# Kernel tuning notes

Measured on AMD Instinct MI355X. Metric: run time of the kernel, lower is better.

The kernel has to match this reference:

```python
import jax, jax.numpy as jnp
import numpy as np

D_MODEL, D_K, D_V, H = 512, 64, 64, 8
B, NQ, NK = 16, 784, 784
HW = 28  # sqrt(NQ)


def setup_inputs() -> dict:
    key = jax.random.key(0)
    ks = jax.random.split(key, 12)
    std = 0.001  # torch init.normal_(weight, std=0.001)
    return {
        "queries": jax.random.normal(ks[0], (B, NQ, D_MODEL), jnp.float32),
        "keys": jax.random.normal(ks[1], (B, NK, D_MODEL), jnp.float32),
        "values": jax.random.normal(ks[2], (B, NK, D_MODEL), jnp.float32),
        "self_corr": jax.random.normal(ks[3], (B, 1, NQ, NK), jnp.float32),
        # weights stored [in, out] for x @ W
        "Wq": jax.random.normal(ks[4], (D_MODEL, H * D_K), jnp.float32) * std,
        "bq": jnp.zeros((H * D_K,), jnp.float32),
        "Wk": jax.random.normal(ks[5], (D_MODEL, H * D_K), jnp.float32) * std,
        "bk": jnp.zeros((H * D_K,), jnp.float32),
        "Wv": jax.random.normal(ks[6], (D_MODEL, H * D_V), jnp.float32) * std,
        "bv": jnp.zeros((H * D_V,), jnp.float32),
        "Wo": jax.random.normal(ks[7], (H * D_V, D_MODEL), jnp.float32) * std,
        "bo": jnp.zeros((D_MODEL,), jnp.float32),
    }


def reference(queries, keys, values, self_corr, Wq, bq, Wk, bk, Wv, bv, Wo, bo):
    b, nq, cc = queries.shape
    nk = keys.shape[1]
    # projections -> [b, h, n, d]
    q = (queries @ Wq + bq).reshape(b, nq, H, D_K).transpose(0, 2, 1, 3)
    k = (keys @ Wk + bk).reshape(b, nk, H, D_K).transpose(0, 2, 1, 3)
    v = (values @ Wv + bv).reshape(b, nk, H, D_V).transpose(0, 2, 1, 3)
    # scaled scores [b, h, nq, nk]
    att_qk = jnp.einsum("bhqd,bhkd->bhqk", q, k) / np.sqrt(D_K).astype(np.float32)
    enhanced = att_qk + self_corr.reshape(b, -1, nq, nk)  # additive bias (broadcast over heads)
    attn = jax.nn.softmax(enhanced, axis=-1)
    # dropout is identity at inference (reference in eval mode)
    ctx = jnp.einsum("bhqk,bhkd->bhqd", attn, v)
    ctx = ctx.transpose(0, 2, 1, 3).reshape(b, nq, H * D_V)
    out = ctx @ Wo + bo  # [b, nq, d_model]
    hw = int(np.sqrt(nq))
    return out.transpose(0, 2, 1).reshape(b, cc, hw, hw)
```

## Files before the change

kernel.cpp:

```cpp
#include <hip/hip_runtime.h>

#define SZX ((size_t)12544 * 512)
#define WSEG ((size_t)262144)

typedef __attribute__((ext_vector_type(8))) short short8;
typedef __attribute__((ext_vector_type(4))) short short4s;
typedef __attribute__((ext_vector_type(4))) float floatx4;

typedef const __attribute__((address_space(1))) void* gas_cvp;
typedef __attribute__((address_space(3))) void* las_vp;

__device__ __forceinline__ void gl_lds16(const void* g, void* l) {
    __builtin_amdgcn_global_load_lds((gas_cvp)g, (las_vp)l, 16, 0, 0);
}

__device__ __forceinline__ unsigned short f2bf(float f) {
    unsigned int u = __float_as_uint(f);
    u += 0x7fffu + ((u >> 16) & 1u);
    return (unsigned short)(u >> 16);
}

__device__ __forceinline__ short8 cvt8(floatx4 a, floatx4 b) {
    short8 r;
    r[0] = (short)f2bf(a[0]); r[1] = (short)f2bf(a[1]);
    r[2] = (short)f2bf(a[2]); r[3] = (short)f2bf(a[3]);
    r[4] = (short)f2bf(b[0]); r[5] = (short)f2bf(b[1]);
    r[6] = (short)f2bf(b[2]); r[7] = (short)f2bf(b[3]);
    return r;
}

__device__ __forceinline__ short8 lds_read8(const unsigned short* p) {
    short4s a = *(const short4s*)p;
    short4s b = *(const short4s*)(p + 4);
    return __builtin_shufflevector(a, b, 0, 1, 2, 3, 4, 5, 6, 7);
}

#define MFMA16(a, b, c) __builtin_amdgcn_mfma_f32_16x16x32_bf16(a, b, c, 0, 0, 0)

__global__ void transpose_cvt(const float* __restrict__ W0, const float* __restrict__ W1,
                              const float* __restrict__ W2, const float* __restrict__ W3,
                              unsigned short* __restrict__ out) {
    __shared__ float tile[32][33];
    const float* W = blockIdx.z == 0 ? W0 : blockIdx.z == 1 ? W1 : blockIdx.z == 2 ? W2 : W3;
    unsigned short* O = out + (size_t)blockIdx.z * WSEG;
    int x = blockIdx.x * 32 + threadIdx.x;
    int y0 = blockIdx.y * 32;
    for (int k = threadIdx.y; k < 32; k += 8)
        tile[k][threadIdx.x] = W[(size_t)(y0 + k) * 512 + x];
    __syncthreads();
    int xo = blockIdx.y * 32 + threadIdx.x;
    int yo0 = blockIdx.x * 32;
    for (int k = threadIdx.y; k < 32; k += 8)
        O[(size_t)(yo0 + k) * 512 + xo] = f2bf(tile[threadIdx.x][k]);
}

__global__ __launch_bounds__(256) void gemm_qkv(
    const float* __restrict__ Xq, const float* __restrict__ Xk,
    const float* __restrict__ Xv, const unsigned short* __restrict__ Wt,
    const float* __restrict__ bq, const float* __restrict__ bk, const float* __restrict__ bv,
    unsigned short* __restrict__ Qb, unsigned short* __restrict__ Kb,
    unsigned short* __restrict__ Vtb)
{
    __shared__ float Xls[128 * 32];
    __shared__ unsigned short Wls[128 * 32];
    int z = blockIdx.z;
    const float* X = z == 0 ? Xq : z == 1 ? Xk : Xv;
    const unsigned short* Wz = Wt + (size_t)z * WSEG;
    const float* bias = z == 0 ? bq : z == 1 ? bk : bv;

    int tid = threadIdx.x;
    int lane = tid & 63, wave = tid >> 6;
    int wm = wave & 1, wn = wave >> 1;
    int c16 = lane & 15, g = lane >> 4;

    const float* Xbase = X + (size_t)blockIdx.x * 128 * 512;
    const unsigned short* Wbase = Wz + (size_t)blockIdx.y * 128 * 512;
    int tm = (z < 2) ? blockIdx.x : blockIdx.y;
    int tn = (z < 2) ? blockIdx.y : blockIdx.x;
    int wx = (z < 2) ? wm : wn;
    int ww = (z < 2) ? wn : wm;

    floatx4 acc[4][4];
#pragma unroll
    for (int i = 0; i < 4; i++)
#pragma unroll
        for (int j = 0; j < 4; j++) acc[i][j] = (floatx4){0.f, 0.f, 0.f, 0.f};

    for (int kb = 0; kb < 16; ++kb) {
        int k0 = kb * 32;
#pragma unroll
        for (int rep = 0; rep < 4; ++rep) {
            int slot = rep * 256 + tid;
            int row = slot >> 3, kp = slot & 7;
            int src = kp ^ (row & 7);
            gl_lds16(Xbase + (size_t)row * 512 + k0 + src * 4, &Xls[slot * 4]);
        }
#pragma unroll
        for (int rep = 0; rep < 2; ++rep) {
            int slot = rep * 256 + tid;
            int row = slot >> 2, kp = slot & 3;
            gl_lds16(Wbase + (size_t)row * 512 + k0 + kp * 8, &Wls[slot * 8]);
        }
        __syncthreads();

        short8 xf[4], wf[4];
#pragma unroll
        for (int i = 0; i < 4; i++) {
            int row = wx * 64 + i * 16 + c16;
            int sw = row & 7;
            floatx4 a = *(const floatx4*)&Xls[row * 32 + ((2 * g + 0) ^ sw) * 4];
            floatx4 b2 = *(const floatx4*)&Xls[row * 32 + ((2 * g + 1) ^ sw) * 4];
            xf[i] = cvt8(a, b2);
        }
#pragma unroll
        for (int j = 0; j < 4; j++)
            wf[j] = *(const short8*)&Wls[(ww * 64 + j * 16 + c16) * 32 + g * 8];

        if (z < 2) {
#pragma unroll
            for (int i = 0; i < 4; i++)
#pragma unroll
                for (int j = 0; j < 4; j++)
                    acc[i][j] = MFMA16(xf[i], wf[j], acc[i][j]);
        } else {
#pragma unroll
            for (int i = 0; i < 4; i++)
#pragma unroll
                for (int j = 0; j < 4; j++)
                    acc[i][j] = MFMA16(wf[i], xf[j], acc[i][j]);
        }
        __syncthreads();
    }

#pragma unroll
    for (int j = 0; j < 4; j++) {
        int n = tn * 128 + wn * 64 + j * 16 + c16;
        int bi = n / 784, nn = n - bi * 784;
        float bvn = (z < 2) ? bias[n] : 0.f;
#pragma unroll
        for (int i = 0; i < 4; i++) {
#pragma unroll
            for (int r4 = 0; r4 < 4; r4++) {
                int m = tm * 128 + wm * 64 + i * 16 + g * 4 + r4;
                float v = acc[i][j][r4] + ((z < 2) ? bvn : bias[m]);
                if (z == 0)      Qb[(size_t)m * 512 + n] = f2bf(v);
                else if (z == 1) Kb[(size_t)m * 512 + n] = f2bf(v);
                else {
                    int h = m >> 6, d = m & 63;
                    Vtb[(((size_t)bi * 8 + h) * 64 + d) * 784 + nn] = f2bf(v);
                }
            }
        }
    }
}

__global__ __launch_bounds__(256) void gemm_out(
    const unsigned short* __restrict__ Wto, const unsigned short* __restrict__ ctx,
    const float* __restrict__ bo, float* __restrict__ out)
{
    __shared__ unsigned short Als[64 * 32];
    __shared__ unsigned short Bls[128 * 32];
    int tid = threadIdx.x;
    int lane = tid & 63, wn = tid >> 6;
    int c16 = lane & 15, g = lane >> 4;
    int tm = blockIdx.x, tn = blockIdx.y;

    const unsigned short* Abase = Wto + (size_t)tm * 64 * 512;
    const unsigned short* Bbase = ctx + (size_t)tn * 128 * 512;

    floatx4 acc[4][2];
#pragma unroll
    for (int i = 0; i < 4; i++)
#pragma unroll
        for (int j = 0; j < 2; j++) acc[i][j] = (floatx4){0.f, 0.f, 0.f, 0.f};

    for (int kb = 0; kb < 16; ++kb) {
        int k0 = kb * 32;
        {
            int row = tid >> 2, kp = tid & 3;
            gl_lds16(Abase + (size_t)row * 512 + k0 + kp * 8, &Als[tid * 8]);
        }
#pragma unroll
        for (int rep = 0; rep < 2; ++rep) {
            int slot = rep * 256 + tid;
            int row = slot >> 2, kp = slot & 3;
            gl_lds16(Bbase + (size_t)row * 512 + k0 + kp * 8, &Bls[slot * 8]);
        }
        __syncthreads();
        short8 af[4], bfr[2];
#pragma unroll
        for (int i = 0; i < 4; i++)
            af[i] = *(const short8*)&Als[(i * 16 + c16) * 32 + g * 8];
#pragma unroll
        for (int j = 0; j < 2; j++)
            bfr[j] = *(const short8*)&Bls[(wn * 32 + j * 16 + c16) * 32 + g * 8];
#pragma unroll
        for (int i = 0; i < 4; i++)
#pragma unroll
            for (int j = 0; j < 2; j++)
                acc[i][j] = MFMA16(af[i], bfr[j], acc[i][j]);
        __syncthreads();
    }

#pragma unroll
    for (int j = 0; j < 2; j++) {
        int n = tn * 128 + wn * 32 + j * 16 + c16;
        int bi = n / 784, q = n - bi * 784;
#pragma unroll
        for (int i = 0; i < 4; i++) {
#pragma unroll
            for (int r4 = 0; r4 < 4; r4++) {
                int m = tm * 64 + i * 16 + g * 4 + r4;
                out[((size_t)bi * 512 + m) * 784 + q] = acc[i][j][r4] + bo[m];
            }
        }
    }
}

__global__ __launch_bounds__(256) void attn_kernel(
    const unsigned short* __restrict__ Qb,
    const unsigned short* __restrict__ Kb,
    const unsigned short* __restrict__ Vtb,
    const float* __restrict__ corr,
    unsigned short* __restrict__ ctx)
{
    __shared__ unsigned short Plds[2][4][2][16][68];
    int b = blockIdx.x, qt = blockIdx.y, hh = blockIdx.z;
    int tid = threadIdx.x;
    int lane = tid & 63, w = tid >> 6;
    int h = hh * 4 + w;
    int c16 = lane & 15, g = lane >> 4;
    int q0 = qt * 32;

    short8 aq[2][2];
#pragma unroll
    for (int u = 0; u < 2; ++u) {
        int row = q0 + u * 16 + c16; row = row < 784 ? row : 783;
        const unsigned short* qp = Qb + (size_t)(b * 784 + row) * 512 + h * 64 + g * 8;
        aq[u][0] = *(const short8*)qp;
        aq[u][1] = *(const short8*)(qp + 32);
    }

    floatx4 o[2][4];
    float l[2][4];
#pragma unroll
    for (int u = 0; u < 2; ++u)
#pragma unroll
        for (int nt = 0; nt < 4; nt++) { o[u][nt] = (floatx4){0.f, 0.f, 0.f, 0.f}; l[u][nt] = 0.f; }

    const float* corrb = corr + (size_t)b * 784 * 784;
    int crow[2][4];
#pragma unroll
    for (int u = 0; u < 2; ++u)
#pragma unroll
        for (int r = 0; r < 4; ++r) {
            int rr = q0 + u * 16 + g * 4 + r; rr = rr < 784 ? rr : 783;
            crow[u][r] = rr * 784;
        }

    const unsigned short* Vh = Vtb + ((size_t)(b * 8 + h)) * 64 * 784;
    const unsigned short* Kh = Kb + (size_t)b * 784 * 512 + h * 64;

    for (int it = 0; it < 13; ++it) {
        int k0 = it * 64;
        floatx4 s[2][4];
#pragma unroll
        for (int t = 0; t < 4; ++t) {
            int key = k0 + t * 16 + c16; key = key < 784 ? key : 783;
            const unsigned short* kp = Kh + (size_t)key * 512 + g * 8;
            short8 k0f = *(const short8*)kp;
            short8 k1f = *(const short8*)(kp + 32);
#pragma unroll
            for (int u = 0; u < 2; ++u) {
                floatx4 zz = (floatx4){0.f, 0.f, 0.f, 0.f};
                zz = MFMA16(aq[u][0], k0f, zz);
                zz = MFMA16(aq[u][1], k1f, zz);
                s[u][t] = zz;
            }
        }
        unsigned short* pbase = &Plds[it & 1][w][0][0][0];
#pragma unroll
        for (int u = 0; u < 2; ++u)
#pragma unroll
            for (int t = 0; t < 4; ++t) {
                int key = k0 + t * 16 + c16;
                bool valid = key < 784;
                int kc = valid ? key : 783;
#pragma unroll
                for (int r = 0; r < 4; ++r) {
                    float cv = corrb[crow[u][r] + kc];
                    float sv = fmaf(s[u][t][r], 0.125f, cv);
                    float pv = valid ? __expf(sv) : 0.f;
                    l[u][r] += pv;
                    pbase[(u * 16 + g * 4 + r) * 68 + t * 16 + c16] = f2bf(pv);
                }
            }
#pragma unroll
        for (int u = 0; u < 2; ++u) {
            const unsigned short* pr = &Plds[it & 1][w][u][c16][0];
            short8 pa0 = lds_read8(pr + g * 8);
            short8 pa1 = lds_read8(pr + 32 + g * 8);
#pragma unroll
            for (int nt = 0; nt < 4; ++nt) {
                int d = nt * 16 + c16;
                const unsigned short* vp = Vh + (size_t)d * 784 + k0 + g * 8;
                short8 v0 = *(const short8*)vp;
                short8 v1 = *(const short8*)(vp + 32);
                o[u][nt] = MFMA16(pa0, v0, o[u][nt]);
                o[u][nt] = MFMA16(pa1, v1, o[u][nt]);
            }
        }
    }

#pragma unroll
    for (int u = 0; u < 2; ++u)
#pragma unroll
        for (int r = 0; r < 4; ++r) {
            float lv = l[u][r];
            lv += __shfl_xor(lv, 1);
            lv += __shfl_xor(lv, 2);
            lv += __shfl_xor(lv, 4);
            lv += __shfl_xor(lv, 8);
            l[u][r] = 1.0f / lv;
        }
#pragma unroll
    for (int u = 0; u < 2; ++u)
#pragma unroll
        for (int r = 0; r < 4; ++r) {
            int row = q0 + u * 16 + g * 4 + r;
            if (row < 784) {
#pragma unroll
                for (int nt = 0; nt < 4; ++nt)
                    ctx[(size_t)(b * 784 + row) * 512 + h * 64 + nt * 16 + c16] =
                        f2bf(o[u][nt][r] * l[u][r]);
            }
        }
}

extern "C" void kernel_launch(void* const* d_in, const int* in_sizes, int n_in,
                              void* d_out, int out_size, void* d_ws, size_t ws_size,
                              hipStream_t stream) {
    (void)in_sizes; (void)n_in; (void)out_size; (void)ws_size;
    const float* queries = (const float*)d_in[0];
    const float* keys    = (const float*)d_in[1];
    const float* values  = (const float*)d_in[2];
    const float* corr    = (const float*)d_in[3];
    const float* Wq = (const float*)d_in[4];
    const float* bq = (const float*)d_in[5];
    const float* Wk = (const float*)d_in[6];
    const float* bk = (const float*)d_in[7];
    const float* Wv = (const float*)d_in[8];
    const float* bv = (const float*)d_in[9];
    const float* Wo = (const float*)d_in[10];
    const float* bo = (const float*)d_in[11];

    unsigned short* Qb  = (unsigned short*)d_ws;
    unsigned short* Kb  = Qb + SZX;
    unsigned short* Vtb = Kb + SZX;
    unsigned short* ctx = Vtb + SZX;
    unsigned short* Wt  = ctx + SZX;

    transpose_cvt<<<dim3(16, 16, 4), dim3(32, 8), 0, stream>>>(Wq, Wk, Wv, Wo, Wt);
    gemm_qkv<<<dim3(98, 4, 3), 256, 0, stream>>>(queries, keys, values, Wt,
                                                 bq, bk, bv, Qb, Kb, Vtb);
    attn_kernel<<<dim3(16, 25, 2), 256, 0, stream>>>(Qb, Kb, Vtb, corr, ctx);
    gemm_out<<<dim3(8, 98), 256, 0, stream>>>(Wt + 3 * WSEG, ctx, bo, (float*)d_out);
}
```

Before: 335.2 us.

## Double K-tile depth in QKV GEMM and remap blocks for L2 locality

The QKV projection GEMM now stages 64-wide K slices per iteration instead of 32, halving the number of barrier-separated load phases. The W tile gains its own XOR swizzle to avoid LDS bank conflicts. The 2D grid is flattened and remapped so groups of 8 row tiles share the same weight column tiles, aiming for better L2 reuse. Shared memory per block doubles (48 KB), which may lower occupancy.

```diff
diff --git a/kernel.cpp b/kernel.cpp
--- a/kernel.cpp
+++ b/kernel.cpp
@@ -61,8 +61,8 @@
     unsigned short* __restrict__ Qb, unsigned short* __restrict__ Kb,
     unsigned short* __restrict__ Vtb)
 {
-    __shared__ float Xls[128 * 32];
-    __shared__ unsigned short Wls[128 * 32];
+    __shared__ float Xls[128 * 64];
+    __shared__ unsigned short Wls[128 * 64];
     int z = blockIdx.z;
     const float* X = z == 0 ? Xq : z == 1 ? Xk : Xv;
     const unsigned short* Wz = Wt + (size_t)z * WSEG;
@@ -73,10 +73,15 @@
     int wm = wave & 1, wn = wave >> 1;
     int c16 = lane & 15, g = lane >> 4;
 
-    const float* Xbase = X + (size_t)blockIdx.x * 128 * 512;
-    const unsigned short* Wbase = Wz + (size_t)blockIdx.y * 128 * 512;
-    int tm = (z < 2) ? blockIdx.x : blockIdx.y;
-    int tn = (z < 2) ? blockIdx.y : blockIdx.x;
+    int G = blockIdx.x;
+    int i98, i4;
+    if (G < 384) { i98 = (G >> 5) * 8 + (G & 7); i4 = (G >> 3) & 3; }
+    else         { int r = G - 384; i98 = 96 + (r & 1); i4 = r >> 1; }
+
+    const float* Xbase = X + (size_t)i98 * 128 * 512;
+    const unsigned short* Wbase = Wz + (size_t)i4 * 128 * 512;
+    int tm = (z < 2) ? i98 : i4;
+    int tn = (z < 2) ? i4 : i98;
     int wx = (z < 2) ? wm : wn;
     int ww = (z < 2) ? wn : wm;
 
@@ -86,48 +91,57 @@
 #pragma unroll
         for (int j = 0; j < 4; j++) acc[i][j] = (floatx4){0.f, 0.f, 0.f, 0.f};
 
-    for (int kb = 0; kb < 16; ++kb) {
-        int k0 = kb * 32;
+    for (int kb = 0; kb < 8; ++kb) {
+        int k0 = kb * 64;
+#pragma unroll
+        for (int rep = 0; rep < 8; ++rep) {
+            int slot = rep * 256 + tid;
+            int row = slot >> 4, gc = slot & 15;
+            int src = (gc & 8) | ((gc & 7) ^ (row & 7));
+            gl_lds16(Xbase + (size_t)row * 512 + k0 + src * 4, &Xls[slot * 4]);
+        }
 #pragma unroll
         for (int rep = 0; rep < 4; ++rep) {
             int slot = rep * 256 + tid;
-            int row = slot >> 3, kp = slot & 7;
-            int src = kp ^ (row & 7);
-            gl_lds16(Xbase + (size_t)row * 512 + k0 + src * 4, &Xls[slot * 4]);
-        }
-#pragma unroll
-        for (int rep = 0; rep < 2; ++rep) {
-            int slot = rep * 256 + tid;
-            int row = slot >> 2, kp = slot & 3;
-            gl_lds16(Wbase + (size_t)row * 512 + k0 + kp * 8, &Wls[slot * 8]);
+            int row = slot >> 3, gc = slot & 7;
+            int src = gc ^ (row & 7);
+            gl_lds16(Wbase + (size_t)row * 512 + k0 + src * 8, &Wls[slot * 8]);
         }
         __syncthreads();
 
-        short8 xf[4], wf[4];
-#pragma unroll
-        for (int i = 0; i < 4; i++) {
-            int row = wx * 64 + i * 16 + c16;
-            int sw = row & 7;
-            floatx4 a = *(const floatx4*)&Xls[row * 32 + ((2 * g + 0) ^ sw) * 4];
-            floatx4 b2 = *(const floatx4*)&Xls[row * 32 + ((2 * g + 1) ^ sw) * 4];
-            xf[i] = cvt8(a, b2);
-        }
-#pragma unroll
-        for (int j = 0; j < 4; j++)
-            wf[j] = *(const short8*)&Wls[(ww * 64 + j * 16 + c16) * 32 + g * 8];
-
-        if (z < 2) {
-#pragma unroll
-            for (int i = 0; i < 4; i++)
-#pragma unroll
-                for (int j = 0; j < 4; j++)
-                    acc[i][j] = MFMA16(xf[i], wf[j], acc[i][j]);
-        } else {
-#pragma unroll
-            for (int i = 0; i < 4; i++)
-#pragma unroll
-                for (int j = 0; j < 4; j++)
-                    acc[i][j] = MFMA16(wf[i], xf[j], acc[i][j]);
+#pragma unroll
+        for (int kk = 0; kk < 2; ++kk) {
+            short8 xf[4], wf[4];
+#pragma unroll
+            for (int i = 0; i < 4; i++) {
+                int row = wx * 64 + i * 16 + c16;
+                int sw = row & 7;
+                int g0 = kk * 8 + 2 * g;
+                int p0 = (g0 & 8) | ((g0 & 7) ^ sw);
+                int p1 = ((g0 + 1) & 8) | (((g0 + 1) & 7) ^ sw);
+                floatx4 a  = *(const floatx4*)&Xls[row * 64 + p0 * 4];
+                floatx4 b2 = *(const floatx4*)&Xls[row * 64 + p1 * 4];
+                xf[i] = cvt8(a, b2);
+            }
+#pragma unroll
+            for (int j = 0; j < 4; j++) {
+                int row = ww * 64 + j * 16 + c16;
+                int gl = kk * 4 + g;
+                wf[j] = *(const short8*)&Wls[row * 64 + (gl ^ (row & 7)) * 8];
+            }
+            if (z < 2) {
+#pragma unroll
+                for (int i = 0; i < 4; i++)
+#pragma unroll
+                    for (int j = 0; j < 4; j++)
+                        acc[i][j] = MFMA16(xf[i], wf[j], acc[i][j]);
+            } else {
+#pragma unroll
+                for (int i = 0; i < 4; i++)
+#pragma unroll
+                    for (int j = 0; j < 4; j++)
+                        acc[i][j] = MFMA16(wf[i], xf[j], acc[i][j]);
+            }
         }
         __syncthreads();
     }
@@ -361,8 +375,8 @@
     unsigned short* Wt  = ctx + SZX;
 
     transpose_cvt<<<dim3(16, 16, 4), dim3(32, 8), 0, stream>>>(Wq, Wk, Wv, Wo, Wt);
-    gemm_qkv<<<dim3(98, 4, 3), 256, 0, stream>>>(queries, keys, values, Wt,
-                                                 bq, bk, bv, Qb, Kb, Vtb);
+    gemm_qkv<<<dim3(392, 1, 3), 256, 0, stream>>>(queries, keys, values, Wt,
+                                                  bq, bk, bv, Qb, Kb, Vtb);
     attn_kernel<<<dim3(16, 25, 2), 256, 0, stream>>>(Qb, Kb, Vtb, corr, ctx);
     gemm_out<<<dim3(8, 98), 256, 0, stream>>>(Wt + 3 * WSEG, ctx, bo, (float*)d_out);
 }
```

Measured after the change: 322.4 us. 3.8% less time.
